# Optimization experiments

Measured on AMD Instinct MI355X. Metric: run time of the kernel, lower is better.

The kernel has to match this reference:

```python
import jax, jax.numpy as jnp
import numpy as np

N = 20000
E = 640000
R = 8          # num_rels == num_bases (basis regularizer with num_bases=-1)
B = 8
IN_SIZE = 128
HID = 256      # 4 * fea_dimen
FEA = 64
TIME = 2880
POI = 12


def setup_inputs() -> dict:
    key = jax.random.key(0)
    ks = jax.random.split(key, 20)
    s = 0.02
    inp = {
        'src': jax.random.randint(ks[0], (E,), 0, N),
        'dst': jax.random.randint(ks[1], (E,), 0, N),
        'etype': jax.random.randint(ks[2], (E,), 0, R),
        'poi_distribution': jax.random.normal(ks[3], (N, POI), jnp.float32),
        'time_distribution': jax.random.normal(ks[4], (N, TIME), jnp.float32),
        'road_feature': jax.random.normal(ks[5], (N, IN_SIZE), jnp.float32),
        # input projections
        'poi_w': jax.random.normal(ks[6], (POI, FEA), jnp.float32) * s,
        'poi_b': jnp.zeros((FEA,), jnp.float32),
        'time_w': jax.random.normal(ks[7], (TIME, 2 * FEA), jnp.float32) * s,
        'time_b': jnp.zeros((2 * FEA,), jnp.float32),
        'road_w': jax.random.normal(ks[8], (IN_SIZE, FEA), jnp.float32) * s,
        'road_b': jnp.zeros((FEA,), jnp.float32),
        # RelGraphConv layer 1 (basis decomposition)
        'basis1': jax.random.normal(ks[9], (B, HID, HID), jnp.float32) * s,
        'coef1': jax.random.normal(ks[10], (R, B), jnp.float32) * s,
        'loop_w1': jax.random.normal(ks[11], (HID, HID), jnp.float32) * s,
        'bias1': jnp.zeros((HID,), jnp.float32),
        # RelGraphConv layer 2
        'basis2': jax.random.normal(ks[12], (B, HID, HID), jnp.float32) * s,
        'coef2': jax.random.normal(ks[13], (R, B), jnp.float32) * s,
        'loop_w2': jax.random.normal(ks[14], (HID, HID), jnp.float32) * s,
        'bias2': jnp.zeros((HID,), jnp.float32),
    }
    return inp


def _rel_graph_conv(h, src, dst, etype, basis, coef, loop_w, bias):
    # W_r = sum_b coef[r,b] * basis[b]  -> (R, HID, HID), small
    W = jnp.einsum('rb,bio->rio', coef, basis)
    # transform every node by every relation weight, then gather per edge
    y = jnp.einsum('ni,rio->nro', h, W)          # (N, R, HID)
    msgs = y[src, etype]                          # (E, HID) gather
    agg = jax.ops.segment_sum(msgs, dst, num_segments=h.shape[0])  # scatter-sum
    return agg + h @ loop_w + bias


def reference(src, dst, etype, poi_distribution, time_distribution, road_feature,
              poi_w, poi_b, time_w, time_b, road_w, road_b,
              basis1, coef1, loop_w1, bias1, basis2, coef2, loop_w2, bias2):
    poi_feat = poi_distribution @ poi_w + poi_b       # (N, 64)
    time_feat = time_distribution @ time_w + time_b   # (N, 128)
    road_feat = road_feature @ road_w + road_b        # (N, 64)
    feat = jnp.concatenate([poi_feat, time_feat, road_feat], axis=1)  # (N, 256)
    h = _rel_graph_conv(feat, src, dst, etype, basis1, coef1, loop_w1, bias1)
    h = jax.nn.relu(h)  # dropout=0.0 -> identity
    h = _rel_graph_conv(h, src, dst, etype, basis2, coef2, loop_w2, bias2)
    return h
```

## Files before the change

### kernel.cpp

```cpp
#include <hip/hip_runtime.h>

#define NN 20000
#define NE 640000
#define NR 8
#define NB 8
#define HID 256
#define KPOI 12
#define KTIME 2880
#define KROAD 128
#define NK (NN * NR)
#define SPLITK 5
#define KCH (KTIME / SPLITK)

typedef __attribute__((ext_vector_type(8))) short bf8_t;
typedef __attribute__((ext_vector_type(4))) float f4_t;

__device__ inline unsigned short f2bf(float f) {
  unsigned int u = __float_as_uint(f);
  u += 0x7FFF + ((u >> 16) & 1);
  return (unsigned short)(u >> 16);
}
__device__ inline float bf2f(unsigned short h) {
  return __uint_as_float((unsigned int)h << 16);
}

__global__ __launch_bounds__(256) void make_WT12(
    const float* __restrict__ coef1, const float* __restrict__ basis1,
    const float* __restrict__ coef2, const float* __restrict__ basis2,
    unsigned short* __restrict__ WT) {
  int idx = blockIdx.x * 256 + threadIdx.x;
  int r = idx >> 16;
  int o = (idx >> 8) & 255;
  int i = idx & 255;
  const float* coef  = (r < NR) ? coef1 : coef2;
  const float* basis = (r < NR) ? basis1 : basis2;
  int rr = r & 7;
  float acc = 0.f;
#pragma unroll
  for (int b = 0; b < NB; ++b)
    acc += coef[rr * NB + b] * basis[b * HID * HID + i * HID + o];
  WT[idx] = f2bf(acc);
}

__global__ __launch_bounds__(256) void transp_LW(
    const float* __restrict__ w1, const float* __restrict__ w2,
    unsigned short* __restrict__ L1, unsigned short* __restrict__ L2) {
  int idx = blockIdx.x * 256 + threadIdx.x;
  int sel = idx >> 16;
  int j = idx & 65535;
  int r = j >> 8, c = j & 255;
  const float* in = sel ? w2 : w1;
  unsigned short* out = sel ? L2 : L1;
  out[c * HID + r] = f2bf(in[j]);
}

__global__ __launch_bounds__(256) void transp_bf16(const float* __restrict__ in,
                                                   unsigned short* __restrict__ out,
                                                   int R, int Cc) {
  int idx = blockIdx.x * 256 + threadIdx.x;
  if (idx >= R * Cc) return;
  int r = idx / Cc, c = idx - r * Cc;
  out[(size_t)c * R + r] = f2bf(in[idx]);
}

#define BK 16
template<int BM, int BN, int TM, int TN>
__global__ __launch_bounds__(256) void sgemm_bf(
    int M, int Nn, int K,
    const float* __restrict__ A, int lda,
    const float* __restrict__ B, int ldb,
    const float* __restrict__ bias,
    unsigned short* __restrict__ C, int ldc)
{
  constexpr int SA = BM + 4;
  constexpr int SB = BN + 4;
  __shared__ float As[BK * SA];
  __shared__ float Bs[BK * SB];
  const int tid = threadIdx.x;
  const int brow = blockIdx.x * BM;
  const int bcol = blockIdx.y * BN;
  constexpr int TCOLS = BN / TN;
  const int row0 = (tid / TCOLS) * TM;
  const int col0 = (tid % TCOLS) * TN;

  float acc[TM][TN] = {};

  for (int kb = 0; kb < K; kb += BK) {
    constexpr int AIT = (BM * 4) / 256;
#pragma unroll
    for (int it = 0; it < AIT; ++it) {
      int i = tid + it * 256;
      int r = i >> 2, q = (i & 3) * 4;
      int grow = brow + r, gk = kb + q;
      if (grow < M && gk + 3 < K) {
        float4 v = *(const float4*)(A + (size_t)grow * lda + gk);
        As[(q + 0) * SA + r] = v.x;
        As[(q + 1) * SA + r] = v.y;
        As[(q + 2) * SA + r] = v.z;
        As[(q + 3) * SA + r] = v.w;
      } else {
#pragma unroll
        for (int j = 0; j < 4; ++j)
          As[(q + j) * SA + r] =
              (grow < M && gk + j < K) ? A[(size_t)grow * lda + gk + j] : 0.f;
      }
    }
    constexpr int BIT = (BN * 4) / 256;
#pragma unroll
    for (int it = 0; it < BIT; ++it) {
      int i = tid + it * 256;
      int k = i / (BN / 4), cq = (i % (BN / 4)) * 4;
      int gk = kb + k, gc = bcol + cq;
      float4 v = {0.f, 0.f, 0.f, 0.f};
      if (gk < K) {
        if (gc + 3 < Nn) {
          v = *(const float4*)(B + (size_t)gk * ldb + gc);
        } else {
#pragma unroll
          for (int j = 0; j < 4; ++j)
            if (gc + j < Nn) (&v.x)[j] = B[(size_t)gk * ldb + gc + j];
        }
      }
      *(float4*)(&Bs[k * SB + cq]) = v;
    }
    __syncthreads();
#pragma unroll
    for (int kk = 0; kk < BK; ++kk) {
      float a[TM], b[TN];
#pragma unroll
      for (int i = 0; i < TM; i += 4)
        *(float4*)(&a[i]) = *(const float4*)(&As[kk * SA + row0 + i]);
#pragma unroll
      for (int j = 0; j < TN; j += 4)
        *(float4*)(&b[j]) = *(const float4*)(&Bs[kk * SB + col0 + j]);
#pragma unroll
      for (int i = 0; i < TM; ++i)
#pragma unroll
        for (int j = 0; j < TN; ++j)
          acc[i][j] += a[i] * b[j];
    }
    __syncthreads();
  }

  float bcache[TN];
#pragma unroll
  for (int j = 0; j < TN; ++j)
    bcache[j] = bias ? bias[bcol + col0 + j] : 0.f;
#pragma unroll
  for (int i = 0; i < TM; ++i) {
    int row = brow + row0 + i;
    if (row >= M) continue;
#pragma unroll
    for (int j = 0; j < TN; ++j) {
      int col = bcol + col0 + j;
      if (col < Nn)
        C[(size_t)row * ldc + col] = f2bf(acc[i][j] + bcache[j]);
    }
  }
}

__global__ __launch_bounds__(256) void mfma_time_sk(
    const float* __restrict__ A,
    const unsigned short* __restrict__ BT,
    float* __restrict__ TP)
{
  __shared__ __align__(16) char ldsA[32 * 128];
  __shared__ __align__(16) char ldsB[128 * 128];
  const int tid = threadIdx.x;
  const int lane = tid & 63;
  const int w = tid >> 6;
  const int brow = blockIdx.x * 32;
  const int kb0 = blockIdx.y * KCH;

  f4_t acc[2][2];
#pragma unroll
  for (int i = 0; i < 2; ++i)
#pragma unroll
    for (int j = 0; j < 2; ++j) acc[i][j] = (f4_t){0.f, 0.f, 0.f, 0.f};

  for (int kb = kb0; kb < kb0 + KCH; kb += 64) {
    {
      int r = tid >> 3, c8 = tid & 7;
      const float* ap = A + (size_t)(brow + r) * KTIME + kb + c8 * 8;
      f4_t v0 = *(const f4_t*)ap;
      f4_t v1 = *(const f4_t*)(ap + 4);
      unsigned short hh[8];
#pragma unroll
      for (int j = 0; j < 4; ++j) { hh[j] = f2bf(v0[j]); hh[4 + j] = f2bf(v1[j]); }
      *(bf8_t*)(ldsA + r * 128 + ((c8 * 16) ^ ((r & 7) << 4))) = *(bf8_t*)hh;
    }
#pragma unroll
    for (int it = 0; it < 4; ++it) {
      int slot = tid + it * 256;
      int r = slot >> 3, c8 = slot & 7;
      bf8_t v = *(const bf8_t*)(BT + (size_t)r * KTIME + kb + c8 * 8);
      *(bf8_t*)(ldsB + r * 128 + ((c8 * 16) ^ ((r & 7) << 4))) = v;
    }
    __syncthreads();
#pragma unroll
    for (int ks = 0; ks < 2; ++ks) {
      const int kbyte = ks * 64 + (lane >> 4) * 16;
      bf8_t af[2], bfr[2];
#pragma unroll
      for (int mi = 0; mi < 2; ++mi) {
        int m = mi * 16 + (lane & 15);
        af[mi] = *(const bf8_t*)(ldsA + m * 128 + (kbyte ^ ((m & 7) << 4)));
      }
#pragma unroll
      for (int ni = 0; ni < 2; ++ni) {
        int n = w * 32 + ni * 16 + (lane & 15);
        bfr[ni] = *(const bf8_t*)(ldsB + n * 128 + (kbyte ^ ((n & 7) << 4)));
      }
#pragma unroll
      for (int mi = 0; mi < 2; ++mi)
#pragma unroll
        for (int ni = 0; ni < 2; ++ni)
          acc[mi][ni] = __builtin_amdgcn_mfma_f32_16x16x32_bf16(
              af[mi], bfr[ni], acc[mi][ni], 0, 0, 0);
    }
    __syncthreads();
  }

  float* tp = TP + (size_t)blockIdx.y * NN * 128;
  const int rq = (lane >> 4) * 4;
  const int cl = lane & 15;
#pragma unroll
  for (int ni = 0; ni < 2; ++ni) {
    int c = w * 32 + ni * 16 + cl;
#pragma unroll
    for (int mi = 0; mi < 2; ++mi) {
#pragma unroll
      for (int j = 0; j < 4; ++j) {
        int row = brow + mi * 16 + rq + j;
        tp[(size_t)row * 128 + c] = acc[mi][ni][j];
      }
    }
  }
}

__global__ __launch_bounds__(256) void time_finish(
    const float* __restrict__ TP, const float* __restrict__ bias,
    unsigned short* __restrict__ featb) {
  int i = blockIdx.x * 256 + threadIdx.x;
  if (i >= NN * 32) return;
  int row = i >> 5, c4 = (i & 31) * 4;
  f4_t s = *(const f4_t*)(TP + (size_t)row * 128 + c4);
#pragma unroll
  for (int k = 1; k < SPLITK; ++k) {
    f4_t v = *(const f4_t*)(TP + (size_t)k * NN * 128 + (size_t)row * 128 + c4);
    s.x += v.x; s.y += v.y; s.z += v.z; s.w += v.w;
  }
  f4_t b = *(const f4_t*)(bias + c4);
  unsigned short h[4] = {f2bf(s.x + b.x), f2bf(s.y + b.y),
                         f2bf(s.z + b.z), f2bf(s.w + b.w)};
  *(ushort4*)(featb + (size_t)row * 256 + 64 + c4) = *(ushort4*)h;
}

__global__ __launch_bounds__(256) void agg_k(
    const int* __restrict__ offs, const unsigned short* __restrict__ ssrc,
    const unsigned short* __restrict__ hin, unsigned short* __restrict__ Z) {
  int w = (blockIdx.x * 256 + threadIdx.x) >> 6;
  int lane = threadIdx.x & 63;
  if (w >= NR * NN) return;
  int q = w / NN;
  int d = w - q * NN;
  int lo = offs[d * NR + q];
  int hi = offs[d * NR + q + 1];
  f4_t az = {0.f, 0.f, 0.f, 0.f};
  int e = lo;
  for (; e + 4 <= hi; e += 4) {
    int s0 = ssrc[e], s1 = ssrc[e + 1], s2 = ssrc[e + 2], s3 = ssrc[e + 3];
    ushort4 u0 = *(const ushort4*)(hin + (size_t)s0 * HID + lane * 4);
    ushort4 u1 = *(const ushort4*)(hin + (size_t)s1 * HID + lane * 4);
    ushort4 u2 = *(const ushort4*)(hin + (size_t)s2 * HID + lane * 4);
    ushort4 u3 = *(const ushort4*)(hin + (size_t)s3 * HID + lane * 4);
    az.x += (bf2f(u0.x) + bf2f(u1.x)) + (bf2f(u2.x) + bf2f(u3.x));
    az.y += (bf2f(u0.y) + bf2f(u1.y)) + (bf2f(u2.y) + bf2f(u3.y));
    az.z += (bf2f(u0.z) + bf2f(u1.z)) + (bf2f(u2.z) + bf2f(u3.z));
    az.w += (bf2f(u0.w) + bf2f(u1.w)) + (bf2f(u2.w) + bf2f(u3.w));
  }
  for (; e < hi; ++e) {
    int s = ssrc[e];
    ushort4 u = *(const ushort4*)(hin + (size_t)s * HID + lane * 4);
    az.x += bf2f(u.x); az.y += bf2f(u.y);
    az.z += bf2f(u.z); az.w += bf2f(u.w);
  }
  unsigned short hz[4] = {f2bf(az.x), f2bf(az.y), f2bf(az.z), f2bf(az.w)};
  *(ushort4*)(Z + (size_t)w * HID + lane * 4) = *(ushort4*)hz;
}

template<int EPI>
__global__ __launch_bounds__(512) void gemm_acc(
    const unsigned short* __restrict__ hbufA,
    const unsigned short* __restrict__ Z,
    const unsigned short* __restrict__ WT,
    const unsigned short* __restrict__ LWT,
    const float* __restrict__ bias,
    float* __restrict__ C, unsigned short* __restrict__ hb)
{
  __shared__ __align__(16) char At[32 * 512];
  __shared__ __align__(16) char Bt[256 * 128];
  const int tid = threadIdx.x;
  const int lane = tid & 63;
  const int w = tid >> 6;
  const int wr = w >> 2;
  const int wc = w & 3;
  const int brow = blockIdx.x * 32;

  f4_t acc[4];
#pragma unroll
  for (int i = 0; i < 4; ++i) acc[i] = (f4_t){0.f, 0.f, 0.f, 0.f};

#pragma unroll 1
  for (int s = 0; s < NR + 1; ++s) {
    const unsigned short* Asrc = (s == 0) ? hbufA : Z + (size_t)(s - 1) * NN * HID;
    const unsigned short* Wsrc = (s == 0) ? LWT : WT + (size_t)(s - 1) * HID * HID;
#pragma unroll
    for (int it = 0; it < 2; ++it) {
      int slot = tid + it * 512;
      int r = slot >> 5, c16 = slot & 31;
      bf8_t v = *(const bf8_t*)(Asrc + (size_t)(brow + r) * HID + c16 * 8);
      *(bf8_t*)(At + r * 512 + ((c16 * 16) ^ ((r & 7) << 4))) = v;
    }
    __syncthreads();
#pragma unroll 1
    for (int kc = 0; kc < 4; ++kc) {
#pragma unroll
      for (int it = 0; it < 4; ++it) {
        int slot = tid + it * 512;
        int n = slot >> 3, c8 = slot & 7;
        bf8_t v = *(const bf8_t*)(Wsrc + (size_t)n * HID + kc * 64 + c8 * 8);
        *(bf8_t*)(Bt + n * 128 + ((c8 * 16) ^ ((n & 7) << 4))) = v;
      }
      __syncthreads();
#pragma unroll
      for (int ks = 0; ks < 2; ++ks) {
        const int kbyte = ks * 64 + (lane >> 4) * 16;
        int m = wr * 16 + (lane & 15);
        bf8_t af = *(const bf8_t*)(
            At + m * 512 + ((kc * 128 + kbyte) ^ ((m & 7) << 4)));
#pragma unroll
        for (int ni = 0; ni < 4; ++ni) {
          int n = wc * 64 + ni * 16 + (lane & 15);
          bf8_t bfr = *(const bf8_t*)(Bt + n * 128 + (kbyte ^ ((n & 7) << 4)));
          acc[ni] = __builtin_amdgcn_mfma_f32_16x16x32_bf16(af, bfr, acc[ni], 0, 0, 0);
        }
      }
      __syncthreads();
    }
  }

  const int rq = (lane >> 4) * 4;
  const int cl = lane & 15;
#pragma unroll
  for (int ni = 0; ni < 4; ++ni) {
    int c = wc * 64 + ni * 16 + cl;
    float bv = bias[c];
#pragma unroll
    for (int j = 0; j < 4; ++j) {
      int row = brow + wr * 16 + rq + j;
      size_t o = (size_t)row * 256 + c;
      float v = acc[ni][j] + bv;
      if (EPI == 0) C[o] = v;
      else          hb[o] = f2bf(fmaxf(v, 0.f));
    }
  }
}

__global__ __launch_bounds__(256) void hist_k(const int* __restrict__ dst,
                                              const int* __restrict__ et,
                                              int* __restrict__ counts) {
  int e = blockIdx.x * 256 + threadIdx.x;
  if (e < NE) atomicAdd(&counts[dst[e] * NR + et[e]], 1);
}

__global__ __launch_bounds__(256) void scan_block(const int* __restrict__ counts,
                                                  int* __restrict__ offs,
                                                  int* __restrict__ bsums) {
  __shared__ int sh[256];
  int base = blockIdx.x * 1024;
  int t = threadIdx.x;
  int v[4];
  int s = 0;
#pragma unroll
  for (int j = 0; j < 4; ++j) {
    int idx = base + t * 4 + j;
    v[j] = (idx < NK) ? counts[idx] : 0;
    s += v[j];
  }
  sh[t] = s;
  __syncthreads();
  for (int off = 1; off < 256; off <<= 1) {
    int x = (t >= off) ? sh[t - off] : 0;
    __syncthreads();
    sh[t] += x;
    __syncthreads();
  }
  int run = sh[t] - s;
#pragma unroll
  for (int j = 0; j < 4; ++j) {
    int idx = base + t * 4 + j;
    if (idx < NK) offs[idx] = run;
    run += v[j];
  }
  if (t == 255) bsums[blockIdx.x] = sh[255];
}

__global__ __launch_bounds__(256) void scan_bsums(int* __restrict__ bsums, int nblk) {
  __shared__ int sh[256];
  int t = threadIdx.x;
  int own = (t < nblk) ? bsums[t] : 0;
  sh[t] = own;
  __syncthreads();
  for (int off = 1; off < 256; off <<= 1) {
    int x = (t >= off) ? sh[t - off] : 0;
    __syncthreads();
    sh[t] += x;
    __syncthreads();
  }
  int ex = sh[t] - own;
  if (t < nblk) bsums[t] = ex;
}

__global__ __launch_bounds__(256) void add_base(int* __restrict__ offs,
                                                const int* __restrict__ bsums,
                                                int* __restrict__ cursor) {
  int idx = blockIdx.x * 256 + threadIdx.x;
  if (idx < NK) {
    int v = offs[idx] + bsums[idx >> 10];
    offs[idx] = v;
    cursor[idx] = v;
  }
  if (idx == NK) offs[NK] = NE;
}

__global__ __launch_bounds__(256) void fill_k(const int* __restrict__ src,
                                              const int* __restrict__ dst,
                                              const int* __restrict__ et,
                                              int* __restrict__ cursor,
                                              unsigned short* __restrict__ ssrc) {
  int e = blockIdx.x * 256 + threadIdx.x;
  if (e < NE) {
    int key = dst[e] * NR + et[e];
    int p = atomicAdd(&cursor[key], 1);
    ssrc[p] = (unsigned short)src[e];
  }
}

extern "C" void kernel_launch(void* const* d_in, const int* in_sizes, int n_in,
                              void* d_out, int out_size, void* d_ws, size_t ws_size,
                              hipStream_t stream) {
  const int*   srcp      = (const int*)d_in[0];
  const int*   dstp      = (const int*)d_in[1];
  const int*   etypep    = (const int*)d_in[2];
  const float* poi_dist  = (const float*)d_in[3];
  const float* time_dist = (const float*)d_in[4];
  const float* road_feat = (const float*)d_in[5];
  const float* poi_w     = (const float*)d_in[6];
  const float* poi_b     = (const float*)d_in[7];
  const float* time_w    = (const float*)d_in[8];
  const float* time_b    = (const float*)d_in[9];
  const float* road_w    = (const float*)d_in[10];
  const float* road_b    = (const float*)d_in[11];
  const float* basis1    = (const float*)d_in[12];
  const float* coef1     = (const float*)d_in[13];
  const float* loop_w1   = (const float*)d_in[14];
  const float* bias1     = (const float*)d_in[15];
  const float* basis2    = (const float*)d_in[16];
  const float* coef2     = (const float*)d_in[17];
  const float* loop_w2   = (const float*)d_in[18];
  const float* bias2     = (const float*)d_in[19];

  float* out = (float*)d_out;

  char* ws = (char*)d_ws;
  unsigned short* WT1    = (unsigned short*)(ws);
  unsigned short* WT2    = (unsigned short*)(ws + 1048576);
  unsigned short* LWT1   = (unsigned short*)(ws + 2097152);
  unsigned short* LWT2   = (unsigned short*)(ws + 2228224);
  unsigned short* TWT    = (unsigned short*)(ws + 2359296);
  unsigned short* hbuf   = (unsigned short*)(ws + 3096576);
  unsigned short* Z      = (unsigned short*)(ws + 13336576);
  float*          TP     = (float*)(ws + 95256576);
  int*            offs   = (int*)  (ws + 146456576);
  int*            bsums  = (int*)  (ws + 147096592);
  unsigned short* ssrc   = (unsigned short*)(ws + 147097616);
  int*            counts = (int*)Z;
  int*            cursor = (int*)TP;

  dim3 blk(256);
  const int MG64 = (NN + 63) / 64;

  hipMemsetAsync(counts, 0, NK * sizeof(int), stream);
  hist_k<<<NE / 256, blk, 0, stream>>>(dstp, etypep, counts);
  scan_block<<<(NK + 1023) / 1024, blk, 0, stream>>>(counts, offs, bsums);
  scan_bsums<<<1, blk, 0, stream>>>(bsums, (NK + 1023) / 1024);
  add_base<<<(NK + 1 + 255) / 256, blk, 0, stream>>>(offs, bsums, cursor);
  fill_k<<<NE / 256, blk, 0, stream>>>(srcp, dstp, etypep, cursor, ssrc);

  transp_LW<<<2 * HID * HID / 256, blk, 0, stream>>>(loop_w1, loop_w2, LWT1, LWT2);
  transp_bf16<<<(KTIME * 128 + 255) / 256, blk, 0, stream>>>(time_w, TWT, KTIME, 128);
  make_WT12<<<2 * NR * HID * HID / 256, blk, 0, stream>>>(coef1, basis1,
                                                          coef2, basis2, WT1);

  sgemm_bf<64, 64, 4, 4><<<dim3(MG64, 1), blk, 0, stream>>>(
      NN, 64, KPOI, poi_dist, KPOI, poi_w, 64, poi_b, hbuf + 0, HID);
  mfma_time_sk<<<dim3(NN / 32, SPLITK), blk, 0, stream>>>(time_dist, TWT, TP);
  time_finish<<<(NN * 32 + 255) / 256, blk, 0, stream>>>(TP, time_b, hbuf);
  sgemm_bf<64, 64, 4, 4><<<dim3(MG64, 1), blk, 0, stream>>>(
      NN, 64, KROAD, road_feat, KROAD, road_w, 64, road_b, hbuf + 192, HID);

  agg_k<<<(NR * NN) / 4, blk, 0, stream>>>(offs, ssrc, hbuf, Z);
  gemm_acc<2><<<NN / 32, 512, 0, stream>>>(hbuf, Z, WT1, LWT1, bias1,
                                           nullptr, hbuf);

  agg_k<<<(NR * NN) / 4, blk, 0, stream>>>(offs, ssrc, hbuf, Z);
  gemm_acc<0><<<NN / 32, 512, 0, stream>>>(hbuf, Z, WT2, LWT2, bias2,
                                           out, nullptr);
}
```

Baseline: 461.6 us.

## Fuse prep and projection kernels, split relation GEMM across two blocks

Merges the three weight-preparation kernels into a single prep kernel. The basis combination now writes through an LDS tile, so both reads and writes are coalesced. The poi and road projections are fused into one launch. The per-layer relation GEMM is split over two grid halves (loop weight plus relations 0-3, and relations 4-7), each writing fp32 partials, and a separate combine kernel adds bias and applies ReLU. This doubles grid parallelism for the main GEMM (625 to 1250 blocks) and cuts launches, at the cost of extra fp32 partial traffic and one more kernel per layer.

```diff
diff --git a/kernel.cpp b/kernel.cpp
--- a/kernel.cpp
+++ b/kernel.cpp
@@ -24,61 +24,75 @@
   return __uint_as_float((unsigned int)h << 16);
 }
 
-__global__ __launch_bounds__(256) void make_WT12(
+__global__ __launch_bounds__(256) void prep_k(
+    const float* __restrict__ loop_w1, const float* __restrict__ loop_w2,
+    const float* __restrict__ time_w,
     const float* __restrict__ coef1, const float* __restrict__ basis1,
     const float* __restrict__ coef2, const float* __restrict__ basis2,
-    unsigned short* __restrict__ WT) {
-  int idx = blockIdx.x * 256 + threadIdx.x;
-  int r = idx >> 16;
-  int o = (idx >> 8) & 255;
-  int i = idx & 255;
-  const float* coef  = (r < NR) ? coef1 : coef2;
-  const float* basis = (r < NR) ? basis1 : basis2;
-  int rr = r & 7;
-  float acc = 0.f;
-#pragma unroll
-  for (int b = 0; b < NB; ++b)
-    acc += coef[rr * NB + b] * basis[b * HID * HID + i * HID + o];
-  WT[idx] = f2bf(acc);
-}
-
-__global__ __launch_bounds__(256) void transp_LW(
-    const float* __restrict__ w1, const float* __restrict__ w2,
-    unsigned short* __restrict__ L1, unsigned short* __restrict__ L2) {
-  int idx = blockIdx.x * 256 + threadIdx.x;
-  int sel = idx >> 16;
-  int j = idx & 65535;
-  int r = j >> 8, c = j & 255;
-  const float* in = sel ? w2 : w1;
-  unsigned short* out = sel ? L2 : L1;
-  out[c * HID + r] = f2bf(in[j]);
-}
-
-__global__ __launch_bounds__(256) void transp_bf16(const float* __restrict__ in,
-                                                   unsigned short* __restrict__ out,
-                                                   int R, int Cc) {
-  int idx = blockIdx.x * 256 + threadIdx.x;
-  if (idx >= R * Cc) return;
-  int r = idx / Cc, c = idx - r * Cc;
-  out[(size_t)c * R + r] = f2bf(in[idx]);
+    unsigned short* __restrict__ LWT1, unsigned short* __restrict__ LWT2,
+    unsigned short* __restrict__ TWT, unsigned short* __restrict__ WT12)
+{
+  __shared__ unsigned short T[64][66];
+  const int b = blockIdx.x;
+  if (b < 512) {
+    int idx = b * 256 + threadIdx.x;
+    int sel = idx >> 16;
+    int j = idx & 65535;
+    int r = j >> 8, c = j & 255;
+    const float* in = sel ? loop_w2 : loop_w1;
+    unsigned short* o = sel ? LWT2 : LWT1;
+    o[c * HID + r] = f2bf(in[j]);
+  } else if (b < 1952) {
+    int idx = (b - 512) * 256 + threadIdx.x;
+    int r = idx >> 7, c = idx & 127;
+    TWT[(size_t)c * KTIME + r] = f2bf(time_w[idx]);
+  } else {
+    const int bid = b - 1952;
+    const int lr = bid >> 4;
+    const int it = (bid >> 2) & 3, ot = bid & 3;
+    const int i0 = it * 64, o0 = ot * 64;
+    const float* coef  = (lr < NR) ? coef1 : coef2;
+    const float* basis = (lr < NR) ? basis1 : basis2;
+    const int r = lr & 7;
+    float cf[NB];
+#pragma unroll
+    for (int q = 0; q < NB; ++q) cf[q] = coef[r * NB + q];
+    const int to = threadIdx.x & 63;
+    const int tq = threadIdx.x >> 6;
+#pragma unroll
+    for (int k = 0; k < 16; ++k) {
+      int i_loc = tq * 16 + k;
+      int i = i0 + i_loc;
+      float acc = 0.f;
+#pragma unroll
+      for (int q = 0; q < NB; ++q)
+        acc += cf[q] * basis[((size_t)(q * HID + i)) * HID + o0 + to];
+      T[i_loc][to] = f2bf(acc);
+    }
+    __syncthreads();
+#pragma unroll
+    for (int k = 0; k < 16; ++k) {
+      int o_loc = tq * 16 + k;
+      WT12[(size_t)lr * HID * HID + (size_t)(o0 + o_loc) * HID + i0 + to] =
+          T[to][o_loc];
+    }
+  }
 }
 
 #define BK 16
-template<int BM, int BN, int TM, int TN>
-__global__ __launch_bounds__(256) void sgemm_bf(
+__device__ inline void sgemm_body(
     int M, int Nn, int K,
     const float* __restrict__ A, int lda,
     const float* __restrict__ B, int ldb,
     const float* __restrict__ bias,
-    unsigned short* __restrict__ C, int ldc)
+    unsigned short* __restrict__ C, int ldc, int brow)
 {
+  constexpr int BM = 64, BN = 64, TM = 4, TN = 4;
   constexpr int SA = BM + 4;
   constexpr int SB = BN + 4;
   __shared__ float As[BK * SA];
   __shared__ float Bs[BK * SB];
   const int tid = threadIdx.x;
-  const int brow = blockIdx.x * BM;
-  const int bcol = blockIdx.y * BN;
   constexpr int TCOLS = BN / TN;
   const int row0 = (tid / TCOLS) * TM;
   const int col0 = (tid % TCOLS) * TN;
@@ -86,10 +100,8 @@
   float acc[TM][TN] = {};
 
   for (int kb = 0; kb < K; kb += BK) {
-    constexpr int AIT = (BM * 4) / 256;
-#pragma unroll
-    for (int it = 0; it < AIT; ++it) {
-      int i = tid + it * 256;
+    {
+      int i = tid;
       int r = i >> 2, q = (i & 3) * 4;
       int grow = brow + r, gk = kb + q;
       if (grow < M && gk + 3 < K) {
@@ -105,20 +117,18 @@
               (grow < M && gk + j < K) ? A[(size_t)grow * lda + gk + j] : 0.f;
       }
     }
-    constexpr int BIT = (BN * 4) / 256;
-#pragma unroll
-    for (int it = 0; it < BIT; ++it) {
-      int i = tid + it * 256;
+    {
+      int i = tid;
       int k = i / (BN / 4), cq = (i % (BN / 4)) * 4;
-      int gk = kb + k, gc = bcol + cq;
+      int gk = kb + k;
       float4 v = {0.f, 0.f, 0.f, 0.f};
       if (gk < K) {
-        if (gc + 3 < Nn) {
-          v = *(const float4*)(B + (size_t)gk * ldb + gc);
+        if (cq + 3 < Nn) {
+          v = *(const float4*)(B + (size_t)gk * ldb + cq);
         } else {
 #pragma unroll
           for (int j = 0; j < 4; ++j)
-            if (gc + j < Nn) (&v.x)[j] = B[(size_t)gk * ldb + gc + j];
+            if (cq + j < Nn) (&v.x)[j] = B[(size_t)gk * ldb + cq + j];
         }
       }
       *(float4*)(&Bs[k * SB + cq]) = v;
@@ -126,37 +136,45 @@
     __syncthreads();
 #pragma unroll
     for (int kk = 0; kk < BK; ++kk) {
-      float a[TM], b[TN];
-#pragma unroll
-      for (int i = 0; i < TM; i += 4)
-        *(float4*)(&a[i]) = *(const float4*)(&As[kk * SA + row0 + i]);
-#pragma unroll
-      for (int j = 0; j < TN; j += 4)
-        *(float4*)(&b[j]) = *(const float4*)(&Bs[kk * SB + col0 + j]);
+      float a[TM], bb[TN];
+      *(float4*)(&a[0]) = *(const float4*)(&As[kk * SA + row0]);
+      *(float4*)(&bb[0]) = *(const float4*)(&Bs[kk * SB + col0]);
 #pragma unroll
       for (int i = 0; i < TM; ++i)
 #pragma unroll
         for (int j = 0; j < TN; ++j)
-          acc[i][j] += a[i] * b[j];
+          acc[i][j] += a[i] * bb[j];
     }
     __syncthreads();
   }
 
   float bcache[TN];
 #pragma unroll
-  for (int j = 0; j < TN; ++j)
-    bcache[j] = bias ? bias[bcol + col0 + j] : 0.f;
+  for (int j = 0; j < TN; ++j) bcache[j] = bias[col0 + j];
 #pragma unroll
   for (int i = 0; i < TM; ++i) {
     int row = brow + row0 + i;
     if (row >= M) continue;
 #pragma unroll
-    for (int j = 0; j < TN; ++j) {
-      int col = bcol + col0 + j;
-      if (col < Nn)
-        C[(size_t)row * ldc + col] = f2bf(acc[i][j] + bcache[j]);
-    }
-  }
+    for (int j = 0; j < TN; ++j)
+      C[(size_t)row * ldc + col0 + j] = f2bf(acc[i][j] + bcache[j]);
+  }
+}
+
+__global__ __launch_bounds__(256) void proj2_k(
+    const float* __restrict__ poi_dist, const float* __restrict__ poi_w,
+    const float* __restrict__ poi_b,
+    const float* __restrict__ road_feat, const float* __restrict__ road_w,
+    const float* __restrict__ road_b,
+    unsigned short* __restrict__ hbuf)
+{
+  const int brow = blockIdx.x * 64;
+  if (blockIdx.y == 0)
+    sgemm_body(NN, 64, KPOI, poi_dist, KPOI, poi_w, 64, poi_b,
+               hbuf + 0, HID, brow);
+  else
+    sgemm_body(NN, 64, KROAD, road_feat, KROAD, road_w, 64, road_b,
+               hbuf + 192, HID, brow);
 }
 
 __global__ __launch_bounds__(256) void mfma_time_sk(
@@ -289,14 +307,12 @@
   *(ushort4*)(Z + (size_t)w * HID + lane * 4) = *(ushort4*)hz;
 }
 
-template<int EPI>
-__global__ __launch_bounds__(512) void gemm_acc(
+__global__ __launch_bounds__(512) void gemm_part(
     const unsigned short* __restrict__ hbufA,
     const unsigned short* __restrict__ Z,
     const unsigned short* __restrict__ WT,
     const unsigned short* __restrict__ LWT,
-    const float* __restrict__ bias,
-    float* __restrict__ C, unsigned short* __restrict__ hb)
+    float* __restrict__ P)
 {
   __shared__ __align__(16) char At[32 * 512];
   __shared__ __align__(16) char Bt[256 * 128];
@@ -306,13 +322,16 @@
   const int wr = w >> 2;
   const int wc = w & 3;
   const int brow = blockIdx.x * 32;
+  const int half = blockIdx.y;
+  const int sbeg = half ? 5 : 0;
+  const int send = half ? 9 : 5;
 
   f4_t acc[4];
 #pragma unroll
   for (int i = 0; i < 4; ++i) acc[i] = (f4_t){0.f, 0.f, 0.f, 0.f};
 
 #pragma unroll 1
-  for (int s = 0; s < NR + 1; ++s) {
+  for (int s = sbeg; s < send; ++s) {
     const unsigned short* Asrc = (s == 0) ? hbufA : Z + (size_t)(s - 1) * NN * HID;
     const unsigned short* Wsrc = (s == 0) ? LWT : WT + (size_t)(s - 1) * HID * HID;
 #pragma unroll
@@ -350,20 +369,39 @@
     }
   }
 
+  float* Pout = P + (size_t)half * NN * HID;
   const int rq = (lane >> 4) * 4;
   const int cl = lane & 15;
 #pragma unroll
   for (int ni = 0; ni < 4; ++ni) {
     int c = wc * 64 + ni * 16 + cl;
-    float bv = bias[c];
 #pragma unroll
     for (int j = 0; j < 4; ++j) {
       int row = brow + wr * 16 + rq + j;
-      size_t o = (size_t)row * 256 + c;
-      float v = acc[ni][j] + bv;
-      if (EPI == 0) C[o] = v;
-      else          hb[o] = f2bf(fmaxf(v, 0.f));
-    }
+      Pout[(size_t)row * HID + c] = acc[ni][j];
+    }
+  }
+}
+
+template<int RELU>
+__global__ __launch_bounds__(256) void combine_k(
+    const float* __restrict__ P, const float* __restrict__ bias,
+    unsigned short* __restrict__ hb, float* __restrict__ C) {
+  int i = blockIdx.x * 256 + threadIdx.x;
+  if (i >= NN * 64) return;
+  int row = i >> 6, c4 = (i & 63) * 4;
+  size_t o = (size_t)row * HID + c4;
+  f4_t a = *(const f4_t*)(P + o);
+  f4_t b = *(const f4_t*)(P + (size_t)NN * HID + o);
+  f4_t bb = *(const f4_t*)(bias + c4);
+  f4_t v = {a.x + b.x + bb.x, a.y + b.y + bb.y,
+            a.z + b.z + bb.z, a.w + b.w + bb.w};
+  if (RELU) {
+    unsigned short h[4] = {f2bf(fmaxf(v.x, 0.f)), f2bf(fmaxf(v.y, 0.f)),
+                           f2bf(fmaxf(v.z, 0.f)), f2bf(fmaxf(v.w, 0.f))};
+    *(ushort4*)(hb + o) = *(ushort4*)h;
+  } else {
+    *(f4_t*)(C + o) = v;
   }
 }
 
@@ -474,8 +512,7 @@
   float* out = (float*)d_out;
 
   char* ws = (char*)d_ws;
-  unsigned short* WT1    = (unsigned short*)(ws);
-  unsigned short* WT2    = (unsigned short*)(ws + 1048576);
+  unsigned short* WT12   = (unsigned short*)(ws);
   unsigned short* LWT1   = (unsigned short*)(ws + 2097152);
   unsigned short* LWT2   = (unsigned short*)(ws + 2228224);
   unsigned short* TWT    = (unsigned short*)(ws + 2359296);
@@ -487,9 +524,12 @@
   unsigned short* ssrc   = (unsigned short*)(ws + 147097616);
   int*            counts = (int*)Z;
   int*            cursor = (int*)TP;
+  float*          P      = TP;
+
+  unsigned short* WT1 = WT12;
+  unsigned short* WT2 = WT12 + (size_t)NR * HID * HID;
 
   dim3 blk(256);
-  const int MG64 = (NN + 63) / 64;
 
   hipMemsetAsync(counts, 0, NK * sizeof(int), stream);
   hist_k<<<NE / 256, blk, 0, stream>>>(dstp, etypep, counts);
@@ -498,23 +538,20 @@
   add_base<<<(NK + 1 + 255) / 256, blk, 0, stream>>>(offs, bsums, cursor);
   fill_k<<<NE / 256, blk, 0, stream>>>(srcp, dstp, etypep, cursor, ssrc);
 
-  transp_LW<<<2 * HID * HID / 256, blk, 0, stream>>>(loop_w1, loop_w2, LWT1, LWT2);
-  transp_bf16<<<(KTIME * 128 + 255) / 256, blk, 0, stream>>>(time_w, TWT, KTIME, 128);
-  make_WT12<<<2 * NR * HID * HID / 256, blk, 0, stream>>>(coef1, basis1,
-                                                          coef2, basis2, WT1);
-
-  sgemm_bf<64, 64, 4, 4><<<dim3(MG64, 1), blk, 0, stream>>>(
-      NN, 64, KPOI, poi_dist, KPOI, poi_w, 64, poi_b, hbuf + 0, HID);
+  prep_k<<<2208, blk, 0, stream>>>(loop_w1, loop_w2, time_w,
+                                   coef1, basis1, coef2, basis2,
+                                   LWT1, LWT2, TWT, WT12);
+
+  proj2_k<<<dim3((NN + 63) / 64, 2), blk, 0, stream>>>(
+      poi_dist, poi_w, poi_b, road_feat, road_w, road_b, hbuf);
   mfma_time_sk<<<dim3(NN / 32, SPLITK), blk, 0, stream>>>(time_dist, TWT, TP);
   time_finish<<<(NN * 32 + 255) / 256, blk, 0, stream>>>(TP, time_b, hbuf);
-  sgemm_bf<64, 64, 4, 4><<<dim3(MG64, 1), blk, 0, stream>>>(
-      NN, 64, KROAD, road_feat, KROAD, road_w, 64, road_b, hbuf + 192, HID);
 
   agg_k<<<(NR * NN) / 4, blk, 0, stream>>>(offs, ssrc, hbuf, Z);
-  gemm_acc<2><<<NN / 32, 512, 0, stream>>>(hbuf, Z, WT1, LWT1, bias1,
-                                           nullptr, hbuf);
+  gemm_part<<<dim3(NN / 32, 2), 512, 0, stream>>>(hbuf, Z, WT1, LWT1, P);
+  combine_k<1><<<(NN * 64 + 255) / 256, blk, 0, stream>>>(P, bias1, hbuf, nullptr);
 
   agg_k<<<(NR * NN) / 4, blk, 0, stream>>>(offs, ssrc, hbuf, Z);
-  gemm_acc<0><<<NN / 32, 512, 0, stream>>>(hbuf, Z, WT2, LWT2, bias2,
-                                           out, nullptr);
-}
+  gemm_part<<<dim3(NN / 32, 2), 512, 0, stream>>>(hbuf, Z, WT2, LWT2, P);
+  combine_k<0><<<(NN * 64 + 255) / 256, blk, 0, stream>>>(P, bias2, nullptr, out);
+}
```

New measurement: 462.1 us. Within noise of the previous version (+0.1%).
